# Kernel tuning notes

Measured on AMD Instinct MI355X. Metric: run time of the kernel, lower is better.

The kernel has to match this reference:

```python
import jax, jax.numpy as jnp
import numpy as np

# config (mirrors init_kwargs)
R = 1.0           # ball-query radius
K = 32            # ball-query neighbors
SPATIAL_STRIDE = 4
TKS = 3           # temporal kernel size (odd)
TPAD = (1, 1)     # replicate temporal padding
HEADS = 8
DIM_HEAD = 64
DIM = 512
MLP = 2048
DEPTH = 2
LN_EPS = 1e-5


def fps(xyz, m):
    # CUDA-style furthest point sampling, starts at index 0. xyz: [N,3] -> [m] int32
    N = xyz.shape[0]
    def body(carry, _):
        dists, last = carry
        d = jnp.sum((xyz - xyz[last]) ** 2, axis=-1)
        dists = jnp.minimum(dists, d)
        nxt = jnp.argmax(dists).astype(jnp.int32)
        return (dists, nxt), nxt
    init = (jnp.full((N,), 1e10, xyz.dtype), jnp.int32(0))
    _, idxs = jax.lax.scan(body, init, None, length=m - 1)
    return jnp.concatenate([jnp.zeros((1,), jnp.int32), idxs])


def ball_query(neighbor_xyz, anchor_xyz):
    # first K neighbor indices within radius R (pad with first found, 0 if none)
    N = neighbor_xyz.shape[0]
    d2 = jnp.sum((anchor_xyz[:, None, :] - neighbor_xyz[None, :, :]) ** 2, -1)  # [M,N]
    cand = jnp.where(d2 < R * R, jnp.arange(N, dtype=jnp.int32)[None, :], N)
    firstk = jnp.sort(cand, axis=-1)[:, :K]
    first = firstk[:, :1]
    idx = jnp.where(firstk >= N, first, firstk)
    return jnp.where(idx >= N, 0, idx).astype(jnp.int32)


def layer_norm(x, g, b):
    mu = jnp.mean(x, -1, keepdims=True)
    var = jnp.var(x, -1, keepdims=True)
    return (x - mu) * jax.lax.rsqrt(var + LN_EPS) * g + b


def p4dconv(xyzs, Wd):
    # tube embedding: FPS anchors + ball-query grouping + 1x1 conv on (dx,dy,dz,dt)
    B, T, N, _ = xyzs.shape
    pad = jnp.concatenate([xyzs[:, :1]] * TPAD[0] + [xyzs] + [xyzs[:, -1:]] * TPAD[1], axis=1)
    Lp = pad.shape[1]
    m = N // SPATIAL_STRIDE
    half = TKS // 2
    new_xyzs, new_feats = [], []
    for t in range(half, Lp - half, 1):  # temporal_stride = 1
        frame = pad[:, t]                                  # [B,N,3]
        aidx = jax.vmap(lambda x: fps(x, m))(frame)        # [B,m]
        anchor = jax.vmap(lambda f, ix: f[ix])(frame, aidx)  # [B,m,3]
        feats_t = []
        for i in range(t - half, t + half + 1):
            nb = pad[:, i]                                 # [B,N,3]
            idx = jax.vmap(ball_query)(nb, anchor)         # [B,m,K]
            grouped = jax.vmap(lambda n, ix: n[ix])(nb, idx)  # [B,m,K,3]
            disp = grouped - anchor[:, :, None, :]
            tdisp = jnp.full((B, m, K, 1), float(i - t), disp.dtype)
            d4 = jnp.concatenate([disp, tdisp], -1)        # [B,m,K,4]
            f = jnp.einsum('bmkf,cf->bmkc', d4, Wd)        # 1x1 conv, no bias/BN/act
            feats_t.append(jnp.max(f, axis=2))             # spatial max pool
        new_feats.append(jnp.max(jnp.stack(feats_t, 1), axis=1))  # temporal max pool
        new_xyzs.append(anchor)
    return jnp.stack(new_xyzs, 1), jnp.stack(new_feats, 1)  # [B,L,m,3], [B,L,m,C]


def attention(xyzs, feats, Wqkv, Wsp, Wout, bout, g, b):
    B, L, n, C = feats.shape
    M = L * n
    x = layer_norm(feats, g, b)
    qkv = jnp.einsum('blnc,ec->blne', x, Wqkv).reshape(B, M, 3, HEADS, DIM_HEAD)
    q, k, v = [jnp.transpose(qkv[:, :, j], (0, 2, 1, 3)) for j in range(3)]  # [B,h,M,d]
    dots = jnp.einsum('bhid,bhjd->bhij', q, k) * (DIM_HEAD ** -0.5)
    attn = jax.nn.softmax(dots, axis=-1)
    out_v = jnp.einsum('bhij,bhjd->bhid', attn, v)
    xyz_f = xyzs.reshape(B, M, 3)
    delta = xyz_f[:, None, :, :] - xyz_f[:, :, None, :]      # [B,i,j,3] = xyz_j - xyz_i
    wdelta = jnp.einsum('bhij,bijc->bhic', attn, delta)      # attn-weighted displacement
    disp_f = jnp.einsum('bhic,dc->bhid', wdelta, Wsp)        # spatial_op Linear(3->d)
    out = out_v + disp_f
    out = jnp.transpose(out, (0, 2, 1, 3)).reshape(B, M, HEADS * DIM_HEAD)
    out = jax.nn.gelu(out @ Wout.T + bout, approximate=False)
    return out.reshape(B, L, n, C) + feats


def feed_forward(x, g, b, W1, b1, W2, b2):
    h = layer_norm(x, g, b)
    h = jax.nn.gelu(h @ W1.T + b1, approximate=False)
    return h @ W2.T + b2 + x


def setup_inputs() -> dict:
    key = jax.random.key(0)
    ks = jax.random.split(key, 12)
    s = 0.02
    inner = HEADS * DIM_HEAD
    return {
        'xyzs': jax.random.normal(ks[0], (2, 4, 1024, 3), jnp.float32),
        'Wd': jax.random.normal(ks[1], (DIM, 4), jnp.float32) * s,
        'Wqkv': jax.random.normal(ks[2], (DEPTH, 3 * inner, DIM), jnp.float32) * s,
        'Wsp': jax.random.normal(ks[3], (DEPTH, DIM_HEAD, 3), jnp.float32) * s,
        'Wout': jax.random.normal(ks[4], (DEPTH, DIM, inner), jnp.float32) * s,
        'bout': jnp.zeros((DEPTH, DIM), jnp.float32),
        'ln1_g': jnp.ones((DEPTH, DIM), jnp.float32),
        'ln1_b': jnp.zeros((DEPTH, DIM), jnp.float32),
        'Wff1': jax.random.normal(ks[5], (DEPTH, MLP, DIM), jnp.float32) * s,
        'bff1': jnp.zeros((DEPTH, MLP), jnp.float32),
        'Wff2': jax.random.normal(ks[6], (DEPTH, DIM, MLP), jnp.float32) * s,
        'bff2': jnp.zeros((DEPTH, DIM), jnp.float32),
        'ln2_g': jnp.ones((DEPTH, DIM), jnp.float32),
        'ln2_b': jnp.zeros((DEPTH, DIM), jnp.float32),
    }


def reference(xyzs, Wd, Wqkv, Wsp, Wout, bout, ln1_g, ln1_b, Wff1, bff1, Wff2, bff2, ln2_g, ln2_b):
    new_xyzs, feats = p4dconv(xyzs, Wd)   # [B,L,m,3], [B,L,m,DIM]
    feats = jax.nn.relu(feats)            # emb_relu after tube embedding
    for i in range(DEPTH):
        feats = attention(new_xyzs, feats, Wqkv[i], Wsp[i], Wout[i], bout[i], ln1_g[i], ln1_b[i])
        feats = feed_forward(feats, ln2_g[i], ln2_b[i], Wff1[i], bff1[i], Wff2[i], bff2[i])
    return feats
```

## Files before the change

kernel.cpp:

```cpp
#include <hip/hip_runtime.h>
#include <math.h>
#include <stdint.h>


typedef __bf16 bf16_t;
typedef __bf16 bf16x8 __attribute__((ext_vector_type(8)));
typedef __bf16 bf16x4 __attribute__((ext_vector_type(4)));
typedef float f32x4 __attribute__((ext_vector_type(4)));

__device__ __forceinline__ void async16(const bf16_t* g, bf16_t* l) {
  __builtin_amdgcn_global_load_lds(
      (const __attribute__((address_space(1))) void*)g,
      (__attribute__((address_space(3))) void*)l, 16, 0, 0);
}

__device__ __forceinline__ float wave_max_dpp(float v) {
  int a = __float_as_int(v);
  int t;
  t = __builtin_amdgcn_update_dpp(a, a, 0x111, 0xf, 0xf, false);
  a = __float_as_int(fmaxf(__int_as_float(a), __int_as_float(t)));
  t = __builtin_amdgcn_update_dpp(a, a, 0x112, 0xf, 0xf, false);
  a = __float_as_int(fmaxf(__int_as_float(a), __int_as_float(t)));
  t = __builtin_amdgcn_update_dpp(a, a, 0x114, 0xf, 0xf, false);
  a = __float_as_int(fmaxf(__int_as_float(a), __int_as_float(t)));
  t = __builtin_amdgcn_update_dpp(a, a, 0x118, 0xf, 0xf, false);
  a = __float_as_int(fmaxf(__int_as_float(a), __int_as_float(t)));
  t = __builtin_amdgcn_update_dpp(a, a, 0x142, 0xf, 0xf, false);
  a = __float_as_int(fmaxf(__int_as_float(a), __int_as_float(t)));
  t = __builtin_amdgcn_update_dpp(a, a, 0x143, 0xf, 0xf, false);
  a = __float_as_int(fmaxf(__int_as_float(a), __int_as_float(t)));
  return __int_as_float(a);
}

template <int CTRL>
__device__ __forceinline__ void tourney(unsigned long long& kv, float& x,
                                        float& y, float& z) {
  uint32_t lo = (uint32_t)kv, hi = (uint32_t)(kv >> 32);
  uint32_t lo2 =
      (uint32_t)__builtin_amdgcn_update_dpp((int)lo, (int)lo, CTRL, 0xf, 0xf, false);
  uint32_t hi2 =
      (uint32_t)__builtin_amdgcn_update_dpp((int)hi, (int)hi, CTRL, 0xf, 0xf, false);
  float x2 = __int_as_float(__builtin_amdgcn_update_dpp(
      __float_as_int(x), __float_as_int(x), CTRL, 0xf, 0xf, false));
  float y2 = __int_as_float(__builtin_amdgcn_update_dpp(
      __float_as_int(y), __float_as_int(y), CTRL, 0xf, 0xf, false));
  float z2 = __int_as_float(__builtin_amdgcn_update_dpp(
      __float_as_int(z), __float_as_int(z), CTRL, 0xf, 0xf, false));
  unsigned long long other = ((unsigned long long)hi2 << 32) | lo2;
  bool take = other > kv;
  kv = take ? other : kv;
  x = take ? x2 : x;
  y = take ? y2 : y;
  z = take ? z2 : z;
}

__global__ __launch_bounds__(512) void fps_kernel(const float* __restrict__ xyzs,
                                                  float* __restrict__ anchors) {
  int bid = blockIdx.x;
  int tid = threadIdx.x;
  int to = bid & 3, b = bid >> 2;
  const float* fr = xyzs + (size_t)(b * 4 + to) * 1024 * 3;
  float* an = anchors + (size_t)(b * 4 + to) * 256 * 3;
  __shared__ __align__(16) float4 cand[2][8];
  __shared__ __align__(16) unsigned long long keys[2][8];
  int w = tid >> 6, lane = tid & 63;
  float px[2], py[2], pz[2], dist[2];
#pragma unroll
  for (int r = 0; r < 2; ++r) {
    int i = r * 512 + tid;
    px[r] = fr[i * 3 + 0]; py[r] = fr[i * 3 + 1]; pz[r] = fr[i * 3 + 2];
    dist[r] = 1e10f;
  }
  float cx = fr[0], cy = fr[1], cz = fr[2];
  if (tid == 0) { an[0] = cx; an[1] = cy; an[2] = cz; }
  for (int s = 1; s < 256; ++s) {
    int par = s & 1;
#pragma unroll
    for (int r = 0; r < 2; ++r) {
      float dx = px[r] - cx, dy = py[r] - cy, dz = pz[r] - cz;
      float d = fmaf(dx, dx, fmaf(dy, dy, dz * dz));
      dist[r] = fminf(dist[r], d);
    }
    float mloc = fmaxf(dist[0], dist[1]);
    float wmax = wave_max_dpp(mloc);
    float smax = __int_as_float(__builtin_amdgcn_readlane(__float_as_int(wmax), 63));
    unsigned int cidx = 0xFFFFFFFFu;
#pragma unroll
    for (int r = 1; r >= 0; --r) {
      unsigned long long m = __ballot(dist[r] == smax);
      unsigned int tz = (unsigned int)__builtin_ctzll(m | 0x8000000000000000ull);
      unsigned int candi = (unsigned int)(r * 512 + w * 64) + tz;
      cidx = m ? candi : cidx;
    }
    unsigned long long key =
        ((unsigned long long)__float_as_uint(smax) << 32) |
        (unsigned long long)(~cidx);
    int wl = (int)(cidx & 63u), rsel = (int)(cidx >> 9);
    if (lane == wl) {
      cand[par][w] = make_float4(rsel ? px[1] : px[0], rsel ? py[1] : py[0],
                                 rsel ? pz[1] : pz[0], 0.0f);
    }
    if (lane == 0) keys[par][w] = key;
    __syncthreads();
    unsigned long long kv = keys[par][lane & 7];
    float4 cd = cand[par][lane & 7];
    float tx = cd.x, ty = cd.y, tz2 = cd.z;
    tourney<0xB1>(kv, tx, ty, tz2);
    tourney<0x4E>(kv, tx, ty, tz2);
    tourney<0x124>(kv, tx, ty, tz2);
    cx = tx; cy = ty; cz = tz2;
    if (tid == 0) { an[s * 3 + 0] = cx; an[s * 3 + 1] = cy; an[s * 3 + 2] = cz; }
  }
}

__global__ __launch_bounds__(256) void conv_cvt_kernel(
    const float* __restrict__ xyzs, const float* __restrict__ anchors,
    const float* __restrict__ Wd, float* __restrict__ feats,
    bf16_t* __restrict__ xln0, const float* __restrict__ g,
    const float* __restrict__ bt,
    const float* __restrict__ s0, bf16_t* __restrict__ d0,
    const float* __restrict__ s1, bf16_t* __restrict__ d1,
    const float* __restrict__ s2, bf16_t* __restrict__ d2,
    const float* __restrict__ s3, bf16_t* __restrict__ d3) {
  int bid = blockIdx.x;
  int tid = threadIdx.x;
  if (bid >= 2048) {
    int base = (bid - 2048) * 256 + tid;
#pragma unroll
    for (int t = 0; t < 3; ++t) {
      int idx = base + t * 524288;
      const float* s; bf16_t* d; int off;
      if (idx < 393216) { s = s0; d = d0; off = idx; }
      else if (idx < 524288) { s = s1; d = d1; off = idx - 393216; }
      else if (idx < 1048576) { s = s2; d = d2; off = idx - 524288; }
      else { s = s3; d = d3; off = idx - 1048576; }
      float4 v = ((const float4*)s)[off];
      bf16x4 o = {(bf16_t)v.x, (bf16_t)v.y, (bf16_t)v.z, (bf16_t)v.w};
      ((bf16x4*)d)[off] = o;
    }
    return;
  }
  int j = bid & 255, to = (bid >> 8) & 3, b = bid >> 10;
  __shared__ float disp[96][4];
  __shared__ int idxbuf[3][32];
  __shared__ float red1[4], red2[4];
  const float* an = anchors + (size_t)((b * 4 + to) * 256 + j) * 3;
  float ax = an[0], ay = an[1], az = an[2];
  int w = tid >> 6, lane = tid & 63;
  if (w < 3) {
    int src = to + w - 1; src = src < 0 ? 0 : (src > 3 ? 3 : src);
    const float* nb = xyzs + (size_t)(b * 4 + src) * 1024 * 3;
    int cnt = 0;
    for (int ch = 0; ch < 16; ++ch) {
      if (cnt >= 32) break;
      int i = ch * 64 + lane;
      float dx = ax - nb[i * 3], dy = ay - nb[i * 3 + 1], dz = az - nb[i * 3 + 2];
      float d2 = dx * dx + dy * dy + dz * dz;
      bool in = d2 < 1.0f;
      unsigned long long mask = __ballot(in);
      if (in) {
        int pos = cnt + (int)__popcll(mask & ((1ull << lane) - 1ull));
        if (pos < 32) idxbuf[w][pos] = i;
      }
      cnt += (int)__popcll(mask);
    }
    if (cnt > 32) cnt = 32;
    if (lane >= cnt && lane < 32) idxbuf[w][lane] = (cnt > 0) ? idxbuf[w][0] : 0;
    if (lane < 32) {
      int ni = idxbuf[w][lane];
      int row = w * 32 + lane;
      disp[row][0] = nb[ni * 3 + 0] - ax;
      disp[row][1] = nb[ni * 3 + 1] - ay;
      disp[row][2] = nb[ni * 3 + 2] - az;
      disp[row][3] = (float)(w - 1);
    }
  }
  __syncthreads();
  int row = (b * 1024) + to * 256 + j;
  const float* wr0 = Wd + tid * 4;
  const float* wr1 = Wd + (tid + 256) * 4;
  float w00 = wr0[0], w01 = wr0[1], w02 = wr0[2], w03 = wr0[3];
  float w10 = wr1[0], w11 = wr1[1], w12 = wr1[2], w13 = wr1[3];
  float mx0 = -1e30f, mx1 = -1e30f;
#pragma unroll 8
  for (int nn = 0; nn < 96; ++nn) {
    float a0 = disp[nn][0], a1 = disp[nn][1], a2 = disp[nn][2], a3 = disp[nn][3];
    mx0 = fmaxf(mx0, a0 * w00 + a1 * w01 + a2 * w02 + a3 * w03);
    mx1 = fmaxf(mx1, a0 * w10 + a1 * w11 + a2 * w12 + a3 * w13);
  }
  float v0 = fmaxf(mx0, 0.0f), v1 = fmaxf(mx1, 0.0f);
  float* fout = feats + (size_t)row * 512;
  fout[tid] = v0;
  fout[tid + 256] = v1;
  float s = v0 + v1;
#pragma unroll
  for (int off = 32; off >= 1; off >>= 1) s += __shfl_xor(s, off, 64);
  if (lane == 0) red1[w] = s;
  __syncthreads();
  float mu = (red1[0] + red1[1] + red1[2] + red1[3]) * (1.0f / 512.0f);
  float dd0 = v0 - mu, dd1 = v1 - mu;
  float q = dd0 * dd0 + dd1 * dd1;
#pragma unroll
  for (int off = 32; off >= 1; off >>= 1) q += __shfl_xor(q, off, 64);
  if (lane == 0) red2[w] = q;
  __syncthreads();
  float var = (red2[0] + red2[1] + red2[2] + red2[3]) * (1.0f / 512.0f);
  float rs = rsqrtf(var + 1e-5f);
  bf16_t* yr = xln0 + (size_t)row * 512;
  yr[tid] = (bf16_t)(dd0 * rs * g[tid] + bt[tid]);
  yr[tid + 256] = (bf16_t)(dd1 * rs * g[tid + 256] + bt[tid + 256]);
}

__global__ __launch_bounds__(256) void ln_kernel(
    const float* __restrict__ x, const float* __restrict__ g,
    const float* __restrict__ bt, bf16_t* __restrict__ y) {
  int row = blockIdx.x;
  int tid = threadIdx.x;
  const float* xr = x + (size_t)row * 512;
  float v0 = xr[tid], v1 = xr[tid + 256];
  float s = v0 + v1;
#pragma unroll
  for (int off = 32; off >= 1; off >>= 1) s += __shfl_xor(s, off, 64);
  __shared__ float red1[4], red2[4];
  int w = tid >> 6, lane = tid & 63;
  if (lane == 0) red1[w] = s;
  __syncthreads();
  float mu = (red1[0] + red1[1] + red1[2] + red1[3]) * (1.0f / 512.0f);
  float d0 = v0 - mu, d1 = v1 - mu;
  float q = d0 * d0 + d1 * d1;
#pragma unroll
  for (int off = 32; off >= 1; off >>= 1) q += __shfl_xor(q, off, 64);
  if (lane == 0) red2[w] = q;
  __syncthreads();
  float var = (red2[0] + red2[1] + red2[2] + red2[3]) * (1.0f / 512.0f);
  float rs = rsqrtf(var + 1e-5f);
  bf16_t* yr = y + (size_t)row * 512;
  yr[tid] = (bf16_t)(d0 * rs * g[tid] + bt[tid]);
  yr[tid + 256] = (bf16_t)(d1 * rs * g[tid + 256] + bt[tid + 256]);
}

template <int BM, int BN, bool GELU, bool BIAS, bool RES, bool OUTBF>
__global__ __launch_bounds__(256) void gemm_bf16(
    const bf16_t* __restrict__ A, const bf16_t* __restrict__ W,
    const float* __restrict__ bias, const float* __restrict__ res,
    void* __restrict__ Cout, int Mn, int Nn, int Kn) {
  constexpr int BK = 64;
  constexpr int WM = BM / 2, WN = BN / 2;
  constexpr int MT = WM / 16, NT = WN / 16;
  constexpr int AIT = (BM * BK / 8) / 256;
  constexpr int BIT = (BN * BK / 8) / 256;
  __shared__ __align__(16) bf16_t As[BM * BK];
  __shared__ __align__(16) bf16_t Bs[BN * BK];
  int tid = threadIdx.x;
  int w = tid >> 6, lane = tid & 63;
  int wr = w >> 1, wc = w & 1;
  int m0 = blockIdx.y * BM, n0 = blockIdx.x * BN;
  int l15 = lane & 15, quad = lane >> 4;
  f32x4 acc[MT][NT] = {};

  const int a_fo = (wr * WM + l15) * BK + quad * 8;
  const int b_fo = (wc * WN + l15) * BK + quad * 8;

  for (int k0 = 0; k0 < Kn; k0 += BK) {
    __syncthreads();
#pragma unroll
    for (int i = 0; i < AIT; ++i) {
      int chunk = i * 256 + tid;
      int row = chunk >> 3, c8 = chunk & 7;
      async16(A + ((size_t)(m0 + row) * Kn + k0 + c8 * 8), As + chunk * 8);
    }
#pragma unroll
    for (int i = 0; i < BIT; ++i) {
      int chunk = i * 256 + tid;
      int row = chunk >> 3, c8 = chunk & 7;
      async16(W + ((size_t)(n0 + row) * Kn + k0 + c8 * 8), Bs + chunk * 8);
    }
    __syncthreads();
#pragma unroll
    for (int ks = 0; ks < 2; ++ks) {
      bf16x8 aF[MT], bF[NT];
#pragma unroll
      for (int mt = 0; mt < MT; ++mt)
        aF[mt] = *(const bf16x8*)&As[a_fo + mt * 16 * BK + ks * 32];
#pragma unroll
      for (int nt = 0; nt < NT; ++nt)
        bF[nt] = *(const bf16x8*)&Bs[b_fo + nt * 16 * BK + ks * 32];
#pragma unroll
      for (int mt = 0; mt < MT; ++mt)
#pragma unroll
        for (int nt = 0; nt < NT; ++nt)
          acc[mt][nt] = __builtin_amdgcn_mfma_f32_16x16x32_bf16(
              aF[mt], bF[nt], acc[mt][nt], 0, 0, 0);
    }
  }
  int rbase = quad * 4;
#pragma unroll
  for (int mt = 0; mt < MT; ++mt) {
#pragma unroll
    for (int reg = 0; reg < 4; ++reg) {
      int r = m0 + wr * WM + mt * 16 + rbase + reg;
      size_t roff = (size_t)r * Nn;
#pragma unroll
      for (int nt = 0; nt < NT; ++nt) {
        int c = n0 + wc * WN + nt * 16 + l15;
        float v = acc[mt][nt][reg];
        if (BIAS) v += bias[c];
        if (GELU) v = v * 0.5f * (1.0f + erff(v * 0.7071067811865475f));
        if (RES) v += res[roff + c];
        if (OUTBF) ((bf16_t*)Cout)[roff + c] = (bf16_t)v;
        else ((float*)Cout)[roff + c] = v;
      }
    }
  }
}

__global__ __launch_bounds__(256) void attn_kernel(
    const bf16_t* __restrict__ qkv, const float* __restrict__ xyzf,
    const float* __restrict__ Wsp, bf16_t* __restrict__ outp) {
  int bid = blockIdx.x;
  int qt = bid & 15, h = (bid >> 4) & 7, b = bid >> 7;
  int tid = threadIdx.x;
  int w = tid >> 6, lane = tid & 63;
  int l15 = lane & 15, quad = lane >> 4;

  __shared__ __align__(16) bf16_t Kb[2][64 * 64];
  __shared__ __align__(16) bf16_t Vt[2][64 * 72];
  __shared__ __align__(16) bf16_t Ps[4][16 * 72];
  __shared__ __align__(16) float4 Xs[2][64];

  const size_t tokbase = (size_t)b * 1024;
  int qbase = qt * 64 + w * 16;

  bf16x8 aQ[2];
  {
    const bf16_t* qp = qkv + (tokbase + qbase + l15) * 1536 + h * 64 + quad * 8;
    aQ[0] = *(const bf16x8*)(qp);
    aQ[1] = *(const bf16x8*)(qp + 32);
  }

  f32x4 oacc[4] = {};
  float lr[4] = {}, pxr[4] = {}, pyr[4] = {}, pzr[4] = {};

  auto stage = [&](int ch, int buf) {
    int j0 = ch * 64;
    int r0 = tid >> 3, seg = tid & 7;
    const bf16_t* g0 = qkv + (tokbase + j0 + r0) * 1536 + 512 + h * 64 + seg * 8;
    async16(g0, Kb[buf] + tid * 8);
    const bf16_t* g1 = qkv + (tokbase + j0 + 32 + r0) * 1536 + 512 + h * 64 + seg * 8;
    async16(g1, Kb[buf] + 2048 + tid * 8);
#pragma unroll
    for (int t = 0; t < 4; ++t) {
      int task = t * 256 + tid;
      int rp = task >> 5, c2 = task & 31;
      const uint32_t* vsrc = (const uint32_t*)(qkv + (tokbase + j0 + 2 * rp) * 1536 +
                                               1024 + h * 64 + 2 * c2);
      uint32_t a = vsrc[0];
      uint32_t bq = vsrc[768];
      uint32_t wlo = (a & 0xffffu) | (bq << 16);
      uint32_t whi = (a >> 16) | (bq & 0xffff0000u);
      uint32_t* vd = (uint32_t*)Vt[buf];
      vd[c2 * 72 + rp] = wlo;
      vd[c2 * 72 + 36 + rp] = whi;
    }
    if (tid < 64) {
      const float* xp = xyzf + (tokbase + j0 + tid) * 3;
      Xs[buf][tid] = make_float4(xp[0], xp[1], xp[2], 0.0f);
    }
  };

  stage(0, 0);
  for (int ch = 0; ch < 16; ++ch) {
    int cur = ch & 1;
    __syncthreads();
    if (ch + 1 < 16) stage(ch + 1, cur ^ 1);
    f32x4 sacc[4] = {};
#pragma unroll
    for (int ks = 0; ks < 2; ++ks)
#pragma unroll
      for (int nt = 0; nt < 4; ++nt) {
        bf16x8 bK = *(const bf16x8*)&Kb[cur][(nt * 16 + l15) * 64 + ks * 32 + quad * 8];
        sacc[nt] = __builtin_amdgcn_mfma_f32_16x16x32_bf16(aQ[ks], bK, sacc[nt], 0, 0, 0);
      }
#pragma unroll
    for (int nt = 0; nt < 4; ++nt) {
      float4 xk = Xs[cur][nt * 16 + l15];
#pragma unroll
      for (int reg = 0; reg < 4; ++reg) {
        float p = __expf(sacc[nt][reg] * 0.125f);
        bf16_t pb = (bf16_t)p;
        float pf = (float)pb;
        Ps[w][(quad * 4 + reg) * 72 + nt * 16 + l15] = pb;
        lr[reg] += pf;
        pxr[reg] = fmaf(pf, xk.x, pxr[reg]);
        pyr[reg] = fmaf(pf, xk.y, pyr[reg]);
        pzr[reg] = fmaf(pf, xk.z, pzr[reg]);
      }
    }
    bf16x8 aP[2];
    aP[0] = *(const bf16x8*)&Ps[w][l15 * 72 + quad * 8];
    aP[1] = *(const bf16x8*)&Ps[w][l15 * 72 + 32 + quad * 8];
#pragma unroll
    for (int ks = 0; ks < 2; ++ks)
#pragma unroll
      for (int ct = 0; ct < 4; ++ct) {
        bf16x8 bV = *(const bf16x8*)&Vt[cur][(ct * 16 + l15) * 72 + ks * 32 + quad * 8];
        oacc[ct] = __builtin_amdgcn_mfma_f32_16x16x32_bf16(aP[ks], bV, oacc[ct], 0, 0, 0);
      }
  }
#pragma unroll
  for (int reg = 0; reg < 4; ++reg) {
#pragma unroll
    for (int off = 1; off <= 8; off <<= 1) {
      lr[reg] += __shfl_xor(lr[reg], off, 64);
      pxr[reg] += __shfl_xor(pxr[reg], off, 64);
      pyr[reg] += __shfl_xor(pyr[reg], off, 64);
      pzr[reg] += __shfl_xor(pzr[reg], off, 64);
    }
  }
#pragma unroll
  for (int reg = 0; reg < 4; ++reg) {
    size_t tok = tokbase + qbase + quad * 4 + reg;
    float inv = 1.0f / lr[reg];
    const float* xqp = xyzf + tok * 3;
    float wd0 = pxr[reg] * inv - xqp[0];
    float wd1 = pyr[reg] * inv - xqp[1];
    float wd2 = pzr[reg] * inv - xqp[2];
#pragma unroll
    for (int ct = 0; ct < 4; ++ct) {
      int c = ct * 16 + l15;
      const float* wr = Wsp + c * 3;
      float dv = wd0 * wr[0] + wd1 * wr[1] + wd2 * wr[2];
      outp[tok * 512 + h * 64 + c] = (bf16_t)(oacc[ct][reg] * inv + dv);
    }
  }
}

extern "C" void kernel_launch(void* const* d_in, const int* in_sizes, int n_in,
                              void* d_out, int out_size, void* d_ws, size_t ws_size,
                              hipStream_t stream) {
  const float* xyzs = (const float*)d_in[0];
  const float* Wd   = (const float*)d_in[1];
  const float* Wqkv = (const float*)d_in[2];
  const float* Wsp  = (const float*)d_in[3];
  const float* Wout = (const float*)d_in[4];
  const float* bout = (const float*)d_in[5];
  const float* ln1g = (const float*)d_in[6];
  const float* ln1b = (const float*)d_in[7];
  const float* Wff1 = (const float*)d_in[8];
  const float* bff1 = (const float*)d_in[9];
  const float* Wff2 = (const float*)d_in[10];
  const float* bff2 = (const float*)d_in[11];
  const float* ln2g = (const float*)d_in[12];
  const float* ln2b = (const float*)d_in[13];
  float* out = (float*)d_out;

  float* ws = (float*)d_ws;
  float* anchors = ws;
  float* featsA  = ws + 8192;
  float* featsB  = featsA + 1048576;
  float* big     = featsB + 1048576;
  bf16_t* bigb   = (bf16_t*)big;
  bf16_t* xlnb   = (bf16_t*)(big + 3145728);
  bf16_t* attob  = xlnb + 1048576;
  bf16_t* wq_b   = attob + 1048576;
  bf16_t* wo_b   = wq_b + 1572864;
  bf16_t* w1_b   = wo_b + 524288;
  bf16_t* w2_b   = w1_b + 2097152;

  fps_kernel<<<8, 512, 0, stream>>>(xyzs, anchors);
  conv_cvt_kernel<<<4096, 256, 0, stream>>>(
      xyzs, anchors, Wd, featsA, xlnb, ln1g, ln1b,
      Wqkv, wq_b, Wout, wo_b, Wff1, w1_b, Wff2, w2_b);

  for (int dep = 0; dep < 2; ++dep) {
    if (dep == 1)
      ln_kernel<<<2048, 256, 0, stream>>>(featsA, ln1g + 512, ln1b + 512, xlnb);
    gemm_bf16<64, 128, false, false, false, true><<<dim3(12, 32), 256, 0, stream>>>(
        xlnb, wq_b + (size_t)dep * 786432, nullptr, nullptr, bigb, 2048, 1536, 512);
    attn_kernel<<<256, 256, 0, stream>>>(bigb, anchors, Wsp + dep * 192, attob);
    gemm_bf16<32, 64, true, true, true, false><<<dim3(8, 64), 256, 0, stream>>>(
        attob, wo_b + (size_t)dep * 262144, bout + dep * 512, featsA, featsB,
        2048, 512, 512);
    ln_kernel<<<2048, 256, 0, stream>>>(featsB, ln2g + dep * 512, ln2b + dep * 512, xlnb);
    gemm_bf16<64, 128, true, true, false, true><<<dim3(16, 32), 256, 0, stream>>>(
        xlnb, w1_b + (size_t)dep * 1048576, bff1 + dep * 2048, nullptr, bigb,
        2048, 2048, 512);
    float* dst = (dep == 1) ? out : featsA;
    gemm_bf16<32, 64, false, true, true, false><<<dim3(8, 64), 256, 0, stream>>>(
        bigb, w2_b + (size_t)dep * 1048576, bff2 + dep * 512, featsB, dst,
        2048, 512, 2048);
  }
}
```

Baseline: 440.8 us.

## Overlap FPS with weight conversion and fetch anchor coordinates from LDS

```diff
diff --git a/kernel.cpp b/kernel.cpp
--- a/kernel.cpp
+++ b/kernel.cpp
@@ -33,113 +33,94 @@
 }
 
 template <int CTRL>
-__device__ __forceinline__ void tourney(unsigned long long& kv, float& x,
-                                        float& y, float& z) {
+__device__ __forceinline__ unsigned long long dpp_max_u64(unsigned long long kv) {
   uint32_t lo = (uint32_t)kv, hi = (uint32_t)(kv >> 32);
   uint32_t lo2 =
       (uint32_t)__builtin_amdgcn_update_dpp((int)lo, (int)lo, CTRL, 0xf, 0xf, false);
   uint32_t hi2 =
       (uint32_t)__builtin_amdgcn_update_dpp((int)hi, (int)hi, CTRL, 0xf, 0xf, false);
-  float x2 = __int_as_float(__builtin_amdgcn_update_dpp(
-      __float_as_int(x), __float_as_int(x), CTRL, 0xf, 0xf, false));
-  float y2 = __int_as_float(__builtin_amdgcn_update_dpp(
-      __float_as_int(y), __float_as_int(y), CTRL, 0xf, 0xf, false));
-  float z2 = __int_as_float(__builtin_amdgcn_update_dpp(
-      __float_as_int(z), __float_as_int(z), CTRL, 0xf, 0xf, false));
   unsigned long long other = ((unsigned long long)hi2 << 32) | lo2;
-  bool take = other > kv;
-  kv = take ? other : kv;
-  x = take ? x2 : x;
-  y = take ? y2 : y;
-  z = take ? z2 : z;
-}
-
-__global__ __launch_bounds__(512) void fps_kernel(const float* __restrict__ xyzs,
-                                                  float* __restrict__ anchors) {
-  int bid = blockIdx.x;
-  int tid = threadIdx.x;
-  int to = bid & 3, b = bid >> 2;
-  const float* fr = xyzs + (size_t)(b * 4 + to) * 1024 * 3;
-  float* an = anchors + (size_t)(b * 4 + to) * 256 * 3;
-  __shared__ __align__(16) float4 cand[2][8];
-  __shared__ __align__(16) unsigned long long keys[2][8];
-  int w = tid >> 6, lane = tid & 63;
-  float px[2], py[2], pz[2], dist[2];
-#pragma unroll
-  for (int r = 0; r < 2; ++r) {
-    int i = r * 512 + tid;
-    px[r] = fr[i * 3 + 0]; py[r] = fr[i * 3 + 1]; pz[r] = fr[i * 3 + 2];
-    dist[r] = 1e10f;
-  }
-  float cx = fr[0], cy = fr[1], cz = fr[2];
-  if (tid == 0) { an[0] = cx; an[1] = cy; an[2] = cz; }
-  for (int s = 1; s < 256; ++s) {
-    int par = s & 1;
-#pragma unroll
-    for (int r = 0; r < 2; ++r) {
-      float dx = px[r] - cx, dy = py[r] - cy, dz = pz[r] - cz;
-      float d = fmaf(dx, dx, fmaf(dy, dy, dz * dz));
-      dist[r] = fminf(dist[r], d);
-    }
-    float mloc = fmaxf(dist[0], dist[1]);
-    float wmax = wave_max_dpp(mloc);
-    float smax = __int_as_float(__builtin_amdgcn_readlane(__float_as_int(wmax), 63));
-    unsigned int cidx = 0xFFFFFFFFu;
-#pragma unroll
-    for (int r = 1; r >= 0; --r) {
-      unsigned long long m = __ballot(dist[r] == smax);
-      unsigned int tz = (unsigned int)__builtin_ctzll(m | 0x8000000000000000ull);
-      unsigned int candi = (unsigned int)(r * 512 + w * 64) + tz;
-      cidx = m ? candi : cidx;
-    }
-    unsigned long long key =
-        ((unsigned long long)__float_as_uint(smax) << 32) |
-        (unsigned long long)(~cidx);
-    int wl = (int)(cidx & 63u), rsel = (int)(cidx >> 9);
-    if (lane == wl) {
-      cand[par][w] = make_float4(rsel ? px[1] : px[0], rsel ? py[1] : py[0],
-                                 rsel ? pz[1] : pz[0], 0.0f);
-    }
-    if (lane == 0) keys[par][w] = key;
-    __syncthreads();
-    unsigned long long kv = keys[par][lane & 7];
-    float4 cd = cand[par][lane & 7];
-    float tx = cd.x, ty = cd.y, tz2 = cd.z;
-    tourney<0xB1>(kv, tx, ty, tz2);
-    tourney<0x4E>(kv, tx, ty, tz2);
-    tourney<0x124>(kv, tx, ty, tz2);
-    cx = tx; cy = ty; cz = tz2;
-    if (tid == 0) { an[s * 3 + 0] = cx; an[s * 3 + 1] = cy; an[s * 3 + 2] = cz; }
-  }
-}
-
-__global__ __launch_bounds__(256) void conv_cvt_kernel(
-    const float* __restrict__ xyzs, const float* __restrict__ anchors,
-    const float* __restrict__ Wd, float* __restrict__ feats,
-    bf16_t* __restrict__ xln0, const float* __restrict__ g,
-    const float* __restrict__ bt,
+  return other > kv ? other : kv;
+}
+
+__global__ __launch_bounds__(512) void fps_cvt_kernel(
+    const float* __restrict__ xyzs, float* __restrict__ anchors,
     const float* __restrict__ s0, bf16_t* __restrict__ d0,
     const float* __restrict__ s1, bf16_t* __restrict__ d1,
     const float* __restrict__ s2, bf16_t* __restrict__ d2,
     const float* __restrict__ s3, bf16_t* __restrict__ d3) {
   int bid = blockIdx.x;
   int tid = threadIdx.x;
-  if (bid >= 2048) {
-    int base = (bid - 2048) * 256 + tid;
-#pragma unroll
-    for (int t = 0; t < 3; ++t) {
-      int idx = base + t * 524288;
-      const float* s; bf16_t* d; int off;
-      if (idx < 393216) { s = s0; d = d0; off = idx; }
-      else if (idx < 524288) { s = s1; d = d1; off = idx - 393216; }
-      else if (idx < 1048576) { s = s2; d = d2; off = idx - 524288; }
-      else { s = s3; d = d3; off = idx - 1048576; }
-      float4 v = ((const float4*)s)[off];
-      bf16x4 o = {(bf16_t)v.x, (bf16_t)v.y, (bf16_t)v.z, (bf16_t)v.w};
-      ((bf16x4*)d)[off] = o;
-    }
+  if (bid >= 8) {
+    int idx = (bid - 8) * 512 + tid;
+    const float* s; bf16_t* d; int off;
+    if (idx < 393216) { s = s0; d = d0; off = idx; }
+    else if (idx < 524288) { s = s1; d = d1; off = idx - 393216; }
+    else if (idx < 1048576) { s = s2; d = d2; off = idx - 524288; }
+    else { s = s3; d = d3; off = idx - 1048576; }
+    float4 v = ((const float4*)s)[off];
+    bf16x4 o = {(bf16_t)v.x, (bf16_t)v.y, (bf16_t)v.z, (bf16_t)v.w};
+    ((bf16x4*)d)[off] = o;
     return;
   }
+  int to = bid & 3, b = bid >> 2;
+  const float* fr = xyzs + (size_t)(b * 4 + to) * 1024 * 3;
+  float* an = anchors + (size_t)(b * 4 + to) * 256 * 3;
+  __shared__ __align__(16) float4 sp[1024];
+  __shared__ __align__(16) unsigned long long keys[2][8];
+  int w = tid >> 6, lane = tid & 63;
+  float px[2], py[2], pz[2], dist[2];
+#pragma unroll
+  for (int r = 0; r < 2; ++r) {
+    int i = r * 512 + tid;
+    float x = fr[i * 3 + 0], y = fr[i * 3 + 1], z = fr[i * 3 + 2];
+    px[r] = x; py[r] = y; pz[r] = z; dist[r] = 1e10f;
+    sp[i] = make_float4(x, y, z, 0.0f);
+  }
+  __syncthreads();
+  float4 c = sp[0];
+  if (tid == 0) { an[0] = c.x; an[1] = c.y; an[2] = c.z; }
+  for (int s = 1; s < 256; ++s) {
+    int par = s & 1;
+#pragma unroll
+    for (int r = 0; r < 2; ++r) {
+      float dx = px[r] - c.x, dy = py[r] - c.y, dz = pz[r] - c.z;
+      float d = fmaf(dx, dx, fmaf(dy, dy, dz * dz));
+      dist[r] = fminf(dist[r], d);
+    }
+    float mloc = fmaxf(dist[0], dist[1]);
+    float wmax = wave_max_dpp(mloc);
+    float smax = __int_as_float(__builtin_amdgcn_readlane(__float_as_int(wmax), 63));
+    unsigned int cidx = 0xFFFFFFFFu;
+#pragma unroll
+    for (int r = 1; r >= 0; --r) {
+      unsigned long long m = __ballot(dist[r] == smax);
+      unsigned int tz = (unsigned int)__builtin_ctzll(m | 0x8000000000000000ull);
+      unsigned int cand = (unsigned int)(r * 512 + w * 64) + tz;
+      cidx = m ? cand : cidx;
+    }
+    unsigned long long key =
+        ((unsigned long long)__float_as_uint(smax) << 32) |
+        (unsigned long long)(~cidx);
+    if (lane == 0) keys[par][w] = key;
+    __syncthreads();
+    unsigned long long kv = keys[par][lane & 7];
+    kv = dpp_max_u64<0xB1>(kv);
+    kv = dpp_max_u64<0x4E>(kv);
+    kv = dpp_max_u64<0x124>(kv);
+    unsigned int bi = ~(unsigned int)(kv & 0xFFFFFFFFull);
+    c = sp[bi];
+    if (tid == 0) { an[s * 3 + 0] = c.x; an[s * 3 + 1] = c.y; an[s * 3 + 2] = c.z; }
+  }
+}
+
+__global__ __launch_bounds__(256) void conv_ln_kernel(
+    const float* __restrict__ xyzs, const float* __restrict__ anchors,
+    const float* __restrict__ Wd, float* __restrict__ feats,
+    bf16_t* __restrict__ xln0, const float* __restrict__ g,
+    const float* __restrict__ bt) {
+  int bid = blockIdx.x;
+  int tid = threadIdx.x;
   int j = bid & 255, to = (bid >> 8) & 3, b = bid >> 10;
   __shared__ float disp[96][4];
   __shared__ int idxbuf[3][32];
@@ -467,10 +448,10 @@
   bf16_t* w1_b   = wo_b + 524288;
   bf16_t* w2_b   = w1_b + 2097152;
 
-  fps_kernel<<<8, 512, 0, stream>>>(xyzs, anchors);
-  conv_cvt_kernel<<<4096, 256, 0, stream>>>(
-      xyzs, anchors, Wd, featsA, xlnb, ln1g, ln1b,
-      Wqkv, wq_b, Wout, wo_b, Wff1, w1_b, Wff2, w2_b);
+  fps_cvt_kernel<<<3080, 512, 0, stream>>>(xyzs, anchors, Wqkv, wq_b, Wout, wo_b,
+                                           Wff1, w1_b, Wff2, w2_b);
+  conv_ln_kernel<<<2048, 256, 0, stream>>>(xyzs, anchors, Wd, featsA, xlnb,
+                                           ln1g, ln1b);
 
   for (int dep = 0; dep < 2; ++dep) {
     if (dep == 1)
```

New measurement: 405.4 us. -8.0%, faster.
